# Performance work log

Measured on AMD Instinct MI355X. Metric: run time of the kernel, lower is better.

Reference implementation:

```python
import jax, jax.numpy as jnp
import numpy as np
from jax import lax

EPS = 1e-5

def _conv(x, w, stride, padding):
    # x: NCHW, w: OIHW
    return lax.conv_general_dilated(
        x, w, window_strides=(stride, stride), padding=padding,
        dimension_numbers=("NCHW", "OIHW", "NCHW"))

def _bn(x, gamma, beta):
    # BatchNorm2d in training mode: batch statistics over (N, H, W)
    mean = jnp.mean(x, axis=(0, 2, 3), keepdims=True)
    var = jnp.var(x, axis=(0, 2, 3), keepdims=True)
    inv = lax.rsqrt(var + EPS)
    g = gamma.reshape(1, -1, 1, 1)
    b = beta.reshape(1, -1, 1, 1)
    return (x - mean) * inv * g + b

def setup_inputs() -> dict:
    key = jax.random.key(0)
    ks = jax.random.split(key, 5)
    B, Cin, H, W = 128, 64, 56, 56
    Cout = 128
    x = jax.random.normal(ks[0], (B, Cin, H, W), dtype=jnp.float32)
    w1 = jax.random.normal(ks[1], (Cout, Cin, 3, 3), dtype=jnp.float32) * 0.05
    w2 = jax.random.normal(ks[2], (Cout, Cout, 3, 3), dtype=jnp.float32) * 0.05
    wd = jax.random.normal(ks[3], (Cout, Cin, 1, 1), dtype=jnp.float32) * 0.05
    g1 = jnp.ones((Cout,), jnp.float32); b1 = jnp.zeros((Cout,), jnp.float32)
    g2 = jnp.ones((Cout,), jnp.float32); b2 = jnp.zeros((Cout,), jnp.float32)
    gd = jnp.ones((Cout,), jnp.float32); bd = jnp.zeros((Cout,), jnp.float32)
    return {"x": x, "w1": w1, "g1": g1, "b1": b1,
            "w2": w2, "g2": g2, "b2": b2,
            "wd": wd, "gd": gd, "bd": bd}

def reference(x, w1, g1, b1, w2, g2, b2, wd, gd, bd):
    stride = 2
    # conv1 (3x3, stride=2, 'same') -> BN -> ReLU
    out = _conv(x, w1, stride, "SAME")
    out = jax.nn.relu(_bn(out, g1, b1))
    # conv2 (3x3, stride=1, 'same') -> BN
    out = _conv(out, w2, 1, "SAME")
    out = _bn(out, g2, b2)
    # downsample identity: 1x1 conv stride=2 'valid' -> BN
    identity = _bn(_conv(x, wd, stride, "VALID"), gd, bd)
    return jax.nn.relu(out + identity)
```

## Files before the change

kernel.cpp:

```cpp
#include <hip/hip_runtime.h>

constexpr int B = 128, Cin = 64, H = 56, W = 56;
constexpr int Cout = 128, Ho = 28, Wo = 28;
constexpr int HW = Ho * Wo;
constexpr int NPIX = B * HW;
constexpr int NOUT = NPIX * Cout;
constexpr int NBLK2 = NPIX / 256;
constexpr float EPS_ = 1e-5f;
constexpr float CNT_ = (float)NPIX;

constexpr int HPX = 57, WPX = 57;
constexpr int HP1 = 30, WP1 = 30;

typedef __attribute__((ext_vector_type(8))) unsigned short u16x8;
typedef __attribute__((ext_vector_type(4))) unsigned short u16x4;
typedef __attribute__((ext_vector_type(8))) short bf16x8;
typedef __attribute__((ext_vector_type(4))) float f32x4;

__device__ inline float bf2f(unsigned short u) {
    union { unsigned int i; float f; } v; v.i = ((unsigned int)u) << 16; return v.f;
}
__device__ inline unsigned short f2bf(float f) {
    union { float f; unsigned int i; } v; v.f = f;
    return (unsigned short)((v.i + 0x7fffu + ((v.i >> 16) & 1u)) >> 16);
}

__device__ inline void gload16(const void* g, void* l) {
    __builtin_amdgcn_global_load_lds(
        (const __attribute__((address_space(1))) unsigned int*)g,
        (__attribute__((address_space(3))) unsigned int*)l, 16, 0, 0);
}

__global__ __launch_bounds__(512) void k_conv2_mfma(
        const unsigned short* __restrict__ xin,
        const unsigned short* __restrict__ wt,
        unsigned short* __restrict__ yout,
        float* __restrict__ part) {
    constexpr int CIN = 128, WP = 30, KTOT = 1152, NSTEP = 36;
    __shared__ unsigned short Alds[3][256 * 32];
    __shared__ unsigned short Blds[3][128 * 32];
    __shared__ float lsum[8][64], lsq[8][64];
    const int tid = threadIdx.x, w = tid >> 6, l = tid & 63;
    const int wr = w >> 1, wc = w & 1;
    const int bid = (blockIdx.x & 7) * (NBLK2 / 8) + (blockIdx.x >> 3);
    const int p0 = bid * 256;
    const char* xb = (const char*)xin;
    const char* wb = (const char*)wt;

    const int sslot = ((l & 3) ^ ((l >> 3) & 3)) * 16;
    const int rswz  = ((l >> 4) ^ ((l >> 1) & 3)) * 16;

    int gA[2], lofsA[2];
    #pragma unroll
    for (int i = 0; i < 2; ++i) {
        int row = w * 32 + i * 16 + (l >> 2);
        int p = p0 + row;
        int n = p / HW, rr = p % HW;
        int oh = rr / Wo, ow = rr % Wo;
        gA[i] = (((n * HP1 + oh) * WP + ow) * CIN) * 2 + sslot;
        lofsA[i] = row * 64 + (l & 3) * 16;
    }
    const int rowb = w * 16 + (l >> 2);
    const int gB = rowb * KTOT * 2 + sslot;
    const int lofsB = rowb * 64 + (l & 3) * 16;

    f32x4 acc[4][4];
    #pragma unroll
    for (int m = 0; m < 4; ++m)
        #pragma unroll
        for (int n = 0; n < 4; ++n)
            acc[m][n] = (f32x4){0.f, 0.f, 0.f, 0.f};

    gload16(xb + gA[0],      (char*)Alds[0] + lofsA[0]);
    gload16(xb + gA[1],      (char*)Alds[0] + lofsA[1]);
    gload16(wb + gB,         (char*)Blds[0] + lofsB);
    gload16(xb + gA[0] + 64, (char*)Alds[1] + lofsA[0]);
    gload16(xb + gA[1] + 64, (char*)Alds[1] + lofsA[1]);
    gload16(wb + gB + 64,    (char*)Blds[1] + lofsB);

    for (int oi = 0; oi < 3; ++oi) {
        const int Abase = oi * WP * CIN * 2;
        #pragma unroll
        for (int u = 0; u < 12; ++u) {
            const int s = oi * 12 + u;
            const int cur = u % 3;
            if (s + 1 < NSTEP) asm volatile("s_waitcnt vmcnt(3)" ::: "memory");
            else               asm volatile("s_waitcnt vmcnt(0)" ::: "memory");
            __builtin_amdgcn_s_barrier();
            if (s + 2 < NSTEP) {
                const int u2 = u + 2;
                const int j2 = u2 >> 2;
                const int c2 = u2 & 3;
                const int koffA = Abase + (j2 == 3 ? WP * CIN * 2 : j2 * CIN * 2) + c2 * 64;
                const int koffB = (s + 2) * 64;
                const int buf = u2 % 3;
                gload16(xb + gA[0] + koffA, (char*)Alds[buf] + lofsA[0]);
                gload16(xb + gA[1] + koffA, (char*)Alds[buf] + lofsA[1]);
                gload16(wb + gB + koffB,    (char*)Blds[buf] + lofsB);
            }
            bf16x8 bf[4];
            #pragma unroll
            for (int n = 0; n < 4; ++n)
                bf[n] = *(const bf16x8*)((const char*)Blds[cur] + (wc * 64 + n * 16 + (l & 15)) * 64 + rswz);
            #pragma unroll
            for (int m = 0; m < 4; ++m) {
                bf16x8 af = *(const bf16x8*)((const char*)Alds[cur] + (wr * 64 + m * 16 + (l & 15)) * 64 + rswz);
                #pragma unroll
                for (int n = 0; n < 4; ++n)
                    acc[m][n] = __builtin_amdgcn_mfma_f32_16x16x32_bf16(af, bf[n], acc[m][n], 0, 0, 0);
            }
        }
    }

    #pragma unroll
    for (int m = 0; m < 4; ++m) {
        int pq = p0 + wr * 64 + m * 16 + (l >> 4) * 4;
        int n = pq / HW, rr = pq % HW;
        #pragma unroll
        for (int q = 0; q < 4; ++q) {
            int co = wc * 64 + q * 16 + (l & 15);
            u16x4 v;
            #pragma unroll
            for (int r = 0; r < 4; ++r) v[r] = f2bf(acc[m][q][r]);
            *(u16x4*)(yout + ((size_t)(n * Cout + co)) * HW + rr) = v;
        }
    }

    float ps[4], pq_[4];
    #pragma unroll
    for (int n = 0; n < 4; ++n) {
        float s_ = 0.f, q_ = 0.f;
        #pragma unroll
        for (int m = 0; m < 4; ++m)
            #pragma unroll
            for (int r = 0; r < 4; ++r) { float v = acc[m][n][r]; s_ += v; q_ += v * v; }
        s_ += __shfl_xor(s_, 16); q_ += __shfl_xor(q_, 16);
        s_ += __shfl_xor(s_, 32); q_ += __shfl_xor(q_, 32);
        ps[n] = s_; pq_[n] = q_;
    }
    __syncthreads();
    if (l < 16) {
        #pragma unroll
        for (int n = 0; n < 4; ++n) { lsum[w][n * 16 + l] = ps[n]; lsq[w][n * 16 + l] = pq_[n]; }
    }
    __syncthreads();
    if (tid < 128) {
        int c = tid, half = c >> 6, j = c & 63;
        float s_ = 0.f, q_ = 0.f;
        #pragma unroll
        for (int r = 0; r < 4; ++r) { s_ += lsum[r * 2 + half][j]; q_ += lsq[r * 2 + half][j]; }
        part[((size_t)bid * 128 + c) * 2]     = s_;
        part[((size_t)bid * 128 + c) * 2 + 1] = q_;
    }
}

__global__ __launch_bounds__(512) void k_conv1_mfma(
        const unsigned short* __restrict__ xin,
        const unsigned short* __restrict__ wt,
        const unsigned short* __restrict__ wtd,
        unsigned short* __restrict__ yout,
        unsigned short* __restrict__ ydout,
        float* __restrict__ part, float* __restrict__ partd) {
    constexpr int CIN = 64, WP = 57, KTOT = 576, NSTEP = 18;
    __shared__ unsigned short Alds[3][256 * 32];
    __shared__ unsigned short Blds[3][128 * 32];
    __shared__ float lsum[8][64], lsq[8][64];
    const int tid = threadIdx.x, w = tid >> 6, l = tid & 63;
    const int wr = w >> 1, wc = w & 1;
    const int bid = (blockIdx.x & 7) * (NBLK2 / 8) + (blockIdx.x >> 3);
    const int p0 = bid * 256;
    const char* xb = (const char*)xin;
    const char* wb = (const char*)wt;

    const int sslot = ((l & 3) ^ ((l >> 3) & 3)) * 16;
    const int rswz  = ((l >> 4) ^ ((l >> 1) & 3)) * 16;

    int gA[2], lofsA[2];
    #pragma unroll
    for (int i = 0; i < 2; ++i) {
        int row = w * 32 + i * 16 + (l >> 2);
        int p = p0 + row;
        int n = p / HW, rr = p % HW;
        int oh = rr / Wo, ow = rr % Wo;
        gA[i] = (((n * HPX + oh * 2) * WP + ow * 2) * CIN) * 2 + sslot;
        lofsA[i] = row * 64 + (l & 3) * 16;
    }
    const int rowb = w * 16 + (l >> 2);
    const int gB = rowb * KTOT * 2 + sslot;
    const int lofsB = rowb * 64 + (l & 3) * 16;

    bf16x8 bd[2][4];
    #pragma unroll
    for (int s = 0; s < 2; ++s)
        #pragma unroll
        for (int n = 0; n < 4; ++n) {
            int co = wc * 64 + n * 16 + (l & 15);
            bd[s][n] = *(const bf16x8*)(wtd + co * 64 + s * 32 + (l >> 4) * 8);
        }

    f32x4 acc[4][4], accd[4][4];
    #pragma unroll
    for (int m = 0; m < 4; ++m)
        #pragma unroll
        for (int n = 0; n < 4; ++n) {
            acc[m][n]  = (f32x4){0.f, 0.f, 0.f, 0.f};
            accd[m][n] = (f32x4){0.f, 0.f, 0.f, 0.f};
        }

    #pragma unroll
    for (int s = 0; s < 2; ++s) {
        gload16(xb + gA[0] + s * 64, (char*)Alds[s] + lofsA[0]);
        gload16(xb + gA[1] + s * 64, (char*)Alds[s] + lofsA[1]);
        gload16(wb + gB + s * 64,    (char*)Blds[s] + lofsB);
    }

    #pragma unroll
    for (int s = 0; s < NSTEP; ++s) {
        const int cur = s % 3;
        if (s + 1 < NSTEP) asm volatile("s_waitcnt vmcnt(3)" ::: "memory");
        else               asm volatile("s_waitcnt vmcnt(0)" ::: "memory");
        __builtin_amdgcn_s_barrier();
        if (s + 2 < NSTEP) {
            const int s2 = s + 2;
            const int seg = s2 >> 1, kh = seg / 3, kw = seg % 3;
            const int koffA = (kh * WP + kw) * CIN * 2 + (s2 & 1) * 64;
            const int koffB = s2 * 64;
            const int buf = s2 % 3;
            gload16(xb + gA[0] + koffA, (char*)Alds[buf] + lofsA[0]);
            gload16(xb + gA[1] + koffA, (char*)Alds[buf] + lofsA[1]);
            gload16(wb + gB + koffB,    (char*)Blds[buf] + lofsB);
        }
        bf16x8 bf[4];
        #pragma unroll
        for (int n = 0; n < 4; ++n)
            bf[n] = *(const bf16x8*)((const char*)Blds[cur] + (wc * 64 + n * 16 + (l & 15)) * 64 + rswz);
        #pragma unroll
        for (int m = 0; m < 4; ++m) {
            bf16x8 af = *(const bf16x8*)((const char*)Alds[cur] + (wr * 64 + m * 16 + (l & 15)) * 64 + rswz);
            #pragma unroll
            for (int n = 0; n < 4; ++n)
                acc[m][n] = __builtin_amdgcn_mfma_f32_16x16x32_bf16(af, bf[n], acc[m][n], 0, 0, 0);
            if (s < 2) {
                #pragma unroll
                for (int n = 0; n < 4; ++n)
                    accd[m][n] = __builtin_amdgcn_mfma_f32_16x16x32_bf16(af, bd[s][n], accd[m][n], 0, 0, 0);
            }
        }
    }

    #pragma unroll
    for (int m = 0; m < 4; ++m) {
        #pragma unroll
        for (int r = 0; r < 4; ++r) {
            int p = p0 + wr * 64 + m * 16 + (l >> 4) * 4 + r;
            int n = p / HW, rr = p % HW;
            int oh = rr / Wo, ow = rr % Wo;
            unsigned short* dst = yout + ((size_t)((n * HP1 + oh + 1) * WP1 + ow + 1)) * 128
                                 + wc * 64 + (l & 15);
            #pragma unroll
            for (int q = 0; q < 4; ++q)
                dst[q * 16] = f2bf(acc[m][q][r]);
        }
    }
    #pragma unroll
    for (int m = 0; m < 4; ++m) {
        int pq = p0 + wr * 64 + m * 16 + (l >> 4) * 4;
        int n = pq / HW, rr = pq % HW;
        #pragma unroll
        for (int q = 0; q < 4; ++q) {
            int co = wc * 64 + q * 16 + (l & 15);
            u16x4 v;
            #pragma unroll
            for (int r = 0; r < 4; ++r) v[r] = f2bf(accd[m][q][r]);
            *(u16x4*)(ydout + ((size_t)(n * Cout + co)) * HW + rr) = v;
        }
    }

    #pragma unroll
    for (int pass = 0; pass < 2; ++pass) {
        f32x4 (&a)[4][4] = pass ? accd : acc;
        float* pt = pass ? partd : part;
        float ps[4], pq_[4];
        #pragma unroll
        for (int n = 0; n < 4; ++n) {
            float s_ = 0.f, q_ = 0.f;
            #pragma unroll
            for (int m = 0; m < 4; ++m)
                #pragma unroll
                for (int r = 0; r < 4; ++r) { float v = a[m][n][r]; s_ += v; q_ += v * v; }
            s_ += __shfl_xor(s_, 16); q_ += __shfl_xor(q_, 16);
            s_ += __shfl_xor(s_, 32); q_ += __shfl_xor(q_, 32);
            ps[n] = s_; pq_[n] = q_;
        }
        __syncthreads();
        if (l < 16) {
            #pragma unroll
            for (int n = 0; n < 4; ++n) { lsum[w][n * 16 + l] = ps[n]; lsq[w][n * 16 + l] = pq_[n]; }
        }
        __syncthreads();
        if (tid < 128) {
            int c = tid, half = c >> 6, j = c & 63;
            float s_ = 0.f, q_ = 0.f;
            #pragma unroll
            for (int r = 0; r < 4; ++r) { s_ += lsum[r * 2 + half][j]; q_ += lsq[r * 2 + half][j]; }
            pt[((size_t)bid * 128 + c) * 2]     = s_;
            pt[((size_t)bid * 128 + c) * 2 + 1] = q_;
        }
    }
}

__global__ __launch_bounds__(256) void k_zerob(unsigned short* __restrict__ xb,
                                               unsigned short* __restrict__ y1p) {
    int idx = blockIdx.x * 256 + threadIdx.x;
    constexpr int NA = B * 113 * 8;
    const u16x8 z = (u16x8){0, 0, 0, 0, 0, 0, 0, 0};
    if (idx < NA) {
        int cg = idx & 7; int t = idx >> 3;
        int bp = t % 113, n = t / 113;
        int ih = bp < 57 ? 56 : bp - 57;
        int iw = bp < 57 ? bp : 56;
        *(u16x8*)(xb + ((size_t)((n * HPX + ih) * WPX + iw)) * Cin + cg * 8) = z;
    } else {
        idx -= NA;
        if (idx >= B * 116 * 16) return;
        int cg = idx & 15; int t = idx >> 4;
        int bp = t % 116, n = t / 116;
        int oh, ow;
        if (bp < 30)      { oh = 0;           ow = bp; }
        else if (bp < 60) { oh = 29;          ow = bp - 30; }
        else if (bp < 88) { oh = bp - 60 + 1; ow = 0; }
        else              { oh = bp - 88 + 1; ow = 29; }
        *(u16x8*)(y1p + ((size_t)((n * HP1 + oh) * WP1 + ow)) * 128 + cg * 8) = z;
    }
}

__global__ __launch_bounds__(512) void k_xprep(const float* __restrict__ x,
                                               unsigned short* __restrict__ xb) {
    __shared__ unsigned short lds[2][64 * 57];
    int n = blockIdx.x / (H / 2), ihp = blockIdx.x % (H / 2), ih0 = ihp * 2;
    const float* src = x + ((size_t)n * Cin * H + ih0) * W;
    for (int j = threadIdx.x; j < 2 * Cin * 14; j += 512) {
        int r = j / 896, rem = j % 896;
        int c = rem / 14, q = rem % 14;
        float4 v = *(const float4*)(src + ((size_t)c * H + r) * W + q * 4);
        unsigned short* d = &lds[r][c * 57 + q * 4];
        d[0] = f2bf(v.x); d[1] = f2bf(v.y); d[2] = f2bf(v.z); d[3] = f2bf(v.w);
    }
    __syncthreads();
    for (int k = threadIdx.x; k < 2 * W * 8; k += 512) {
        int r = k / 448, k2 = k % 448;
        int pix = k2 >> 3, cg = k2 & 7;
        u16x8 v;
        #pragma unroll
        for (int e = 0; e < 8; ++e) v[e] = lds[r][(cg * 8 + e) * 57 + pix];
        *(u16x8*)(xb + ((size_t)((n * HPX + ih0 + r) * WPX + pix)) * Cin + cg * 8) = v;
    }
}

__global__ void k_wprep_all(const float* __restrict__ w1, const float* __restrict__ w2,
                            const float* __restrict__ wd,
                            unsigned short* __restrict__ wt1, unsigned short* __restrict__ wt2,
                            unsigned short* __restrict__ wtd) {
    int idx = blockIdx.x * 256 + threadIdx.x;
    const float* w; unsigned short* wt; int cin, ntap;
    if (idx < 73728)            { w = w1; wt = wt1; cin = 64;  ntap = 9; }
    else if (idx < 73728 + 147456) { idx -= 73728; w = w2; wt = wt2; cin = 128; ntap = 9; }
    else if (idx < 73728 + 147456 + 8192) { idx -= 73728 + 147456; w = wd; wt = wtd; cin = 64; ntap = 1; }
    else return;
    int co = idx / (cin * ntap), r = idx % (cin * ntap);
    int ci = r / ntap, tap = r % ntap;
    wt[co * cin * ntap + tap * cin + ci] = f2bf(w[idx]);
}

__device__ inline void block_reduce2(float& s, float& s2) {
    #pragma unroll
    for (int off = 32; off > 0; off >>= 1) {
        s += __shfl_down(s, off);
        s2 += __shfl_down(s2, off);
    }
    __shared__ float ls[4], ls2[4];
    int wid = threadIdx.x >> 6, lane = threadIdx.x & 63;
    if (lane == 0) { ls[wid] = s; ls2[wid] = s2; }
    __syncthreads();
    if (threadIdx.x == 0) { s = ls[0] + ls[1] + ls[2] + ls[3]; s2 = ls2[0] + ls2[1] + ls2[2] + ls2[3]; }
}

__global__ __launch_bounds__(256) void k_finalize(
        const float* __restrict__ pA, const float* __restrict__ pB, int nA, int nB,
        const float* __restrict__ gA_, const float* __restrict__ bA_,
        const float* __restrict__ gB_, const float* __restrict__ bB_,
        float* __restrict__ scA, float* __restrict__ shA,
        float* __restrict__ scB, float* __restrict__ shB) {
    const bool second = blockIdx.x >= 128;
    const int c = blockIdx.x & 127;
    const float* part = second ? pB : pA;
    const int nblk = second ? nB : nA;
    const float* g = second ? gB_ : gA_;
    const float* b = second ? bB_ : bA_;
    float* scale = second ? scB : scA;
    float* shift = second ? shB : shA;
    float s = 0.f, q = 0.f;
    for (int k = threadIdx.x; k < nblk; k += 256) {
        s += part[((size_t)k * 128 + c) * 2];
        q += part[((size_t)k * 128 + c) * 2 + 1];
    }
    block_reduce2(s, q);
    if (threadIdx.x == 0) {
        float mean = s / CNT_;
        float var = q / CNT_ - mean * mean;
        float inv = rsqrtf(var + EPS_);
        scale[c] = g[c] * inv;
        shift[c] = b[c] - mean * g[c] * inv;
    }
}

__global__ __launch_bounds__(256) void k_bnrelu(unsigned short* __restrict__ y,
        const float* __restrict__ sc, const float* __restrict__ sh) {
    int t = threadIdx.x, cg = t & 15, pl = t >> 4;
    int p = blockIdx.x * 16 + pl;
    int n = p / HW, rr = p % HW;
    int oh = rr / Wo, ow = rr % Wo;
    size_t a = ((size_t)((n * HP1 + oh + 1) * WP1 + ow + 1)) * 128 + cg * 8;
    u16x8 v = *(u16x8*)(y + a);
    u16x8 o;
    #pragma unroll
    for (int e = 0; e < 8; ++e) {
        float f = bf2f(v[e]) * sc[cg * 8 + e] + sh[cg * 8 + e];
        o[e] = f2bf(fmaxf(f, 0.f));
    }
    *(u16x8*)(y + a) = o;
}

__global__ __launch_bounds__(256) void k_final(
        const unsigned short* __restrict__ y2, const unsigned short* __restrict__ yd,
        const float* __restrict__ sc2, const float* __restrict__ sh2,
        const float* __restrict__ scd, const float* __restrict__ shd,
        float* __restrict__ out) {
    int idx = blockIdx.x * 256 + threadIdx.x;
    int plane = idx / (HW / 8);
    int c = plane & (Cout - 1);
    int i = idx % (HW / 8);
    size_t a = (size_t)plane * HW + i * 8;
    u16x8 v2 = *(const u16x8*)(y2 + a);
    u16x8 vd = *(const u16x8*)(yd + a);
    float s2c = sc2[c], h2c = sh2[c], sdc = scd[c], hdc = shd[c];
    float4 r0, r1;
    r0.x = fmaxf(bf2f(v2[0]) * s2c + h2c + bf2f(vd[0]) * sdc + hdc, 0.f);
    r0.y = fmaxf(bf2f(v2[1]) * s2c + h2c + bf2f(vd[1]) * sdc + hdc, 0.f);
    r0.z = fmaxf(bf2f(v2[2]) * s2c + h2c + bf2f(vd[2]) * sdc + hdc, 0.f);
    r0.w = fmaxf(bf2f(v2[3]) * s2c + h2c + bf2f(vd[3]) * sdc + hdc, 0.f);
    r1.x = fmaxf(bf2f(v2[4]) * s2c + h2c + bf2f(vd[4]) * sdc + hdc, 0.f);
    r1.y = fmaxf(bf2f(v2[5]) * s2c + h2c + bf2f(vd[5]) * sdc + hdc, 0.f);
    r1.z = fmaxf(bf2f(v2[6]) * s2c + h2c + bf2f(vd[6]) * sdc + hdc, 0.f);
    r1.w = fmaxf(bf2f(v2[7]) * s2c + h2c + bf2f(vd[7]) * sdc + hdc, 0.f);
    *(float4*)(out + a) = r0;
    *(float4*)(out + a + 4) = r1;
}

extern "C" void kernel_launch(void* const* d_in, const int* in_sizes, int n_in,
                              void* d_out, int out_size, void* d_ws, size_t ws_size,
                              hipStream_t stream) {
    const float* x  = (const float*)d_in[0];
    const float* w1 = (const float*)d_in[1];
    const float* g1 = (const float*)d_in[2];
    const float* b1 = (const float*)d_in[3];
    const float* w2 = (const float*)d_in[4];
    const float* g2 = (const float*)d_in[5];
    const float* b2 = (const float*)d_in[6];
    const float* wd = (const float*)d_in[7];
    const float* gd = (const float*)d_in[8];
    const float* bd = (const float*)d_in[9];
    float* out = (float*)d_out;

    char* ws = (char*)d_ws;
    auto alloc = [&](size_t bytes) { char* p = ws; ws += (bytes + 255) & ~(size_t)255; return p; };
    unsigned short* xb  = (unsigned short*)alloc((size_t)B * HPX * WPX * Cin * 2);
    unsigned short* y1p = (unsigned short*)alloc((size_t)B * HP1 * WP1 * Cout * 2);
    unsigned short* y2b = (unsigned short*)alloc((size_t)NOUT * 2);
    unsigned short* ydb = (unsigned short*)alloc((size_t)NOUT * 2);
    unsigned short* wt1 = (unsigned short*)alloc((size_t)Cout * 576 * 2);
    unsigned short* wt2 = (unsigned short*)alloc((size_t)Cout * 1152 * 2);
    unsigned short* wtd = (unsigned short*)alloc((size_t)Cout * 64 * 2);
    float* part1 = (float*)alloc((size_t)NBLK2 * 128 * 2 * 4);
    float* part2 = (float*)alloc((size_t)NBLK2 * 128 * 2 * 4);
    float* partd = (float*)alloc((size_t)NBLK2 * 128 * 2 * 4);
    float* sc1 = (float*)alloc(128 * 4); float* sh1 = (float*)alloc(128 * 4);
    float* sc2 = (float*)alloc(128 * 4); float* sh2 = (float*)alloc(128 * 4);
    float* scd = (float*)alloc(128 * 4); float* shd = (float*)alloc(128 * 4);

    k_zerob<<<(B * 113 * 8 + B * 116 * 16 + 255) / 256, 256, 0, stream>>>(xb, y1p);
    k_xprep<<<B * (H / 2), 512, 0, stream>>>(x, xb);
    k_wprep_all<<<(73728 + 147456 + 8192 + 255) / 256, 256, 0, stream>>>(w1, w2, wd, wt1, wt2, wtd);

    k_conv1_mfma<<<NBLK2, 512, 0, stream>>>(xb, wt1, wtd, y1p, ydb, part1, partd);

    k_finalize<<<128, 256, 0, stream>>>(part1, part1, NBLK2, NBLK2,
                                        g1, b1, g1, b1, sc1, sh1, sc1, sh1);
    k_bnrelu<<<NPIX / 16, 256, 0, stream>>>(y1p, sc1, sh1);

    k_conv2_mfma<<<NBLK2, 512, 0, stream>>>(y1p, wt2, y2b, part2);

    k_finalize<<<256, 256, 0, stream>>>(part2, partd, NBLK2, NBLK2,
                                        g2, b2, gd, bd, sc2, sh2, scd, shd);

    k_final<<<NOUT / 8 / 256, 256, 0, stream>>>(y2b, ydb, sc2, sh2, scd, shd, out);
}
```

Measured before the change: 164.3 us.

## Raise MFMA wave priority, merge prep kernels, widen elementwise kernels

Wraps the MFMA inner loops of both conv kernels in s_setprio(1)/s_setprio(0), so waves issuing matrix ops get scheduling priority over waves doing loads. Merges the zero-border and weight-prep kernels into one launch to drop a kernel launch. The BN+ReLU and final epilogue kernels now handle 16 elements per thread instead of 8, halving their grid sizes. These are several small independent tweaks, and priority changes can hurt the overlap of loads and compute.

```diff
diff --git a/kernel.cpp b/kernel.cpp
--- a/kernel.cpp
+++ b/kernel.cpp
@@ -102,6 +102,7 @@
             #pragma unroll
             for (int n = 0; n < 4; ++n)
                 bf[n] = *(const bf16x8*)((const char*)Blds[cur] + (wc * 64 + n * 16 + (l & 15)) * 64 + rswz);
+            __builtin_amdgcn_s_setprio(1);
             #pragma unroll
             for (int m = 0; m < 4; ++m) {
                 bf16x8 af = *(const bf16x8*)((const char*)Alds[cur] + (wr * 64 + m * 16 + (l & 15)) * 64 + rswz);
@@ -109,6 +110,7 @@
                 for (int n = 0; n < 4; ++n)
                     acc[m][n] = __builtin_amdgcn_mfma_f32_16x16x32_bf16(af, bf[n], acc[m][n], 0, 0, 0);
             }
+            __builtin_amdgcn_s_setprio(0);
         }
     }
 
@@ -234,6 +236,7 @@
         #pragma unroll
         for (int n = 0; n < 4; ++n)
             bf[n] = *(const bf16x8*)((const char*)Blds[cur] + (wc * 64 + n * 16 + (l & 15)) * 64 + rswz);
+        __builtin_amdgcn_s_setprio(1);
         #pragma unroll
         for (int m = 0; m < 4; ++m) {
             bf16x8 af = *(const bf16x8*)((const char*)Alds[cur] + (wr * 64 + m * 16 + (l & 15)) * 64 + rswz);
@@ -246,6 +249,7 @@
                     accd[m][n] = __builtin_amdgcn_mfma_f32_16x16x32_bf16(af, bd[s][n], accd[m][n], 0, 0, 0);
             }
         }
+        __builtin_amdgcn_s_setprio(0);
     }
 
     #pragma unroll
@@ -309,20 +313,25 @@
     }
 }
 
-__global__ __launch_bounds__(256) void k_zerob(unsigned short* __restrict__ xb,
-                                               unsigned short* __restrict__ y1p) {
+constexpr int NZA = B * 113 * 8;
+constexpr int NZB = B * 116 * 16;
+constexpr int NWP = 73728 + 147456 + 8192;
+__global__ __launch_bounds__(256) void k_prep(
+        unsigned short* __restrict__ xb, unsigned short* __restrict__ y1p,
+        const float* __restrict__ w1, const float* __restrict__ w2,
+        const float* __restrict__ wd,
+        unsigned short* __restrict__ wt1, unsigned short* __restrict__ wt2,
+        unsigned short* __restrict__ wtd) {
     int idx = blockIdx.x * 256 + threadIdx.x;
-    constexpr int NA = B * 113 * 8;
     const u16x8 z = (u16x8){0, 0, 0, 0, 0, 0, 0, 0};
-    if (idx < NA) {
+    if (idx < NZA) {
         int cg = idx & 7; int t = idx >> 3;
         int bp = t % 113, n = t / 113;
         int ih = bp < 57 ? 56 : bp - 57;
         int iw = bp < 57 ? bp : 56;
         *(u16x8*)(xb + ((size_t)((n * HPX + ih) * WPX + iw)) * Cin + cg * 8) = z;
-    } else {
-        idx -= NA;
-        if (idx >= B * 116 * 16) return;
+    } else if (idx < NZA + NZB) {
+        idx -= NZA;
         int cg = idx & 15; int t = idx >> 4;
         int bp = t % 116, n = t / 116;
         int oh, ow;
@@ -331,6 +340,16 @@
         else if (bp < 88) { oh = bp - 60 + 1; ow = 0; }
         else              { oh = bp - 88 + 1; ow = 29; }
         *(u16x8*)(y1p + ((size_t)((n * HP1 + oh) * WP1 + ow)) * 128 + cg * 8) = z;
+    } else {
+        idx -= NZA + NZB;
+        if (idx >= NWP) return;
+        const float* w; unsigned short* wt; int cin, ntap;
+        if (idx < 73728)               { w = w1; wt = wt1; cin = 64;  ntap = 9; }
+        else if (idx < 73728 + 147456) { idx -= 73728; w = w2; wt = wt2; cin = 128; ntap = 9; }
+        else                           { idx -= 73728 + 147456; w = wd; wt = wtd; cin = 64; ntap = 1; }
+        int co = idx / (cin * ntap), r = idx % (cin * ntap);
+        int ci = r / ntap, tap = r % ntap;
+        wt[co * cin * ntap + tap * cin + ci] = f2bf(w[idx]);
     }
 }
 
@@ -355,21 +374,6 @@
         for (int e = 0; e < 8; ++e) v[e] = lds[r][(cg * 8 + e) * 57 + pix];
         *(u16x8*)(xb + ((size_t)((n * HPX + ih0 + r) * WPX + pix)) * Cin + cg * 8) = v;
     }
-}
-
-__global__ void k_wprep_all(const float* __restrict__ w1, const float* __restrict__ w2,
-                            const float* __restrict__ wd,
-                            unsigned short* __restrict__ wt1, unsigned short* __restrict__ wt2,
-                            unsigned short* __restrict__ wtd) {
-    int idx = blockIdx.x * 256 + threadIdx.x;
-    const float* w; unsigned short* wt; int cin, ntap;
-    if (idx < 73728)            { w = w1; wt = wt1; cin = 64;  ntap = 9; }
-    else if (idx < 73728 + 147456) { idx -= 73728; w = w2; wt = wt2; cin = 128; ntap = 9; }
-    else if (idx < 73728 + 147456 + 8192) { idx -= 73728 + 147456; w = wd; wt = wtd; cin = 64; ntap = 1; }
-    else return;
-    int co = idx / (cin * ntap), r = idx % (cin * ntap);
-    int ci = r / ntap, tap = r % ntap;
-    wt[co * cin * ntap + tap * cin + ci] = f2bf(w[idx]);
 }
 
 __device__ inline void block_reduce2(float& s, float& s2) {
@@ -416,19 +420,23 @@
 
 __global__ __launch_bounds__(256) void k_bnrelu(unsigned short* __restrict__ y,
         const float* __restrict__ sc, const float* __restrict__ sh) {
-    int t = threadIdx.x, cg = t & 15, pl = t >> 4;
-    int p = blockIdx.x * 16 + pl;
+    int t = threadIdx.x, cg = t & 7, pl = t >> 3;
+    int p = blockIdx.x * 32 + pl;
     int n = p / HW, rr = p % HW;
     int oh = rr / Wo, ow = rr % Wo;
-    size_t a = ((size_t)((n * HP1 + oh + 1) * WP1 + ow + 1)) * 128 + cg * 8;
-    u16x8 v = *(u16x8*)(y + a);
-    u16x8 o;
+    size_t a = ((size_t)((n * HP1 + oh + 1) * WP1 + ow + 1)) * 128 + cg * 16;
+    u16x8 v0 = *(u16x8*)(y + a);
+    u16x8 v1 = *(u16x8*)(y + a + 8);
+    u16x8 o0, o1;
     #pragma unroll
     for (int e = 0; e < 8; ++e) {
-        float f = bf2f(v[e]) * sc[cg * 8 + e] + sh[cg * 8 + e];
-        o[e] = f2bf(fmaxf(f, 0.f));
-    }
-    *(u16x8*)(y + a) = o;
+        float f0 = bf2f(v0[e]) * sc[cg * 16 + e] + sh[cg * 16 + e];
+        float f1 = bf2f(v1[e]) * sc[cg * 16 + 8 + e] + sh[cg * 16 + 8 + e];
+        o0[e] = f2bf(fmaxf(f0, 0.f));
+        o1[e] = f2bf(fmaxf(f1, 0.f));
+    }
+    *(u16x8*)(y + a) = o0;
+    *(u16x8*)(y + a + 8) = o1;
 }
 
 __global__ __launch_bounds__(256) void k_final(
@@ -436,25 +444,28 @@
         const float* __restrict__ sc2, const float* __restrict__ sh2,
         const float* __restrict__ scd, const float* __restrict__ shd,
         float* __restrict__ out) {
-    int idx = blockIdx.x * 256 + threadIdx.x;
-    int plane = idx / (HW / 8);
+    int u = blockIdx.x * 256 + threadIdx.x;
+    int plane = u / 49;
     int c = plane & (Cout - 1);
-    int i = idx % (HW / 8);
-    size_t a = (size_t)plane * HW + i * 8;
-    u16x8 v2 = *(const u16x8*)(y2 + a);
-    u16x8 vd = *(const u16x8*)(yd + a);
+    int i = u % 49;
+    size_t a = (size_t)plane * HW + i * 16;
     float s2c = sc2[c], h2c = sh2[c], sdc = scd[c], hdc = shd[c];
-    float4 r0, r1;
-    r0.x = fmaxf(bf2f(v2[0]) * s2c + h2c + bf2f(vd[0]) * sdc + hdc, 0.f);
-    r0.y = fmaxf(bf2f(v2[1]) * s2c + h2c + bf2f(vd[1]) * sdc + hdc, 0.f);
-    r0.z = fmaxf(bf2f(v2[2]) * s2c + h2c + bf2f(vd[2]) * sdc + hdc, 0.f);
-    r0.w = fmaxf(bf2f(v2[3]) * s2c + h2c + bf2f(vd[3]) * sdc + hdc, 0.f);
-    r1.x = fmaxf(bf2f(v2[4]) * s2c + h2c + bf2f(vd[4]) * sdc + hdc, 0.f);
-    r1.y = fmaxf(bf2f(v2[5]) * s2c + h2c + bf2f(vd[5]) * sdc + hdc, 0.f);
-    r1.z = fmaxf(bf2f(v2[6]) * s2c + h2c + bf2f(vd[6]) * sdc + hdc, 0.f);
-    r1.w = fmaxf(bf2f(v2[7]) * s2c + h2c + bf2f(vd[7]) * sdc + hdc, 0.f);
-    *(float4*)(out + a) = r0;
-    *(float4*)(out + a + 4) = r1;
+    #pragma unroll
+    for (int hv = 0; hv < 2; ++hv) {
+        u16x8 v2 = *(const u16x8*)(y2 + a + hv * 8);
+        u16x8 vd = *(const u16x8*)(yd + a + hv * 8);
+        float4 r0, r1;
+        r0.x = fmaxf(bf2f(v2[0]) * s2c + h2c + bf2f(vd[0]) * sdc + hdc, 0.f);
+        r0.y = fmaxf(bf2f(v2[1]) * s2c + h2c + bf2f(vd[1]) * sdc + hdc, 0.f);
+        r0.z = fmaxf(bf2f(v2[2]) * s2c + h2c + bf2f(vd[2]) * sdc + hdc, 0.f);
+        r0.w = fmaxf(bf2f(v2[3]) * s2c + h2c + bf2f(vd[3]) * sdc + hdc, 0.f);
+        r1.x = fmaxf(bf2f(v2[4]) * s2c + h2c + bf2f(vd[4]) * sdc + hdc, 0.f);
+        r1.y = fmaxf(bf2f(v2[5]) * s2c + h2c + bf2f(vd[5]) * sdc + hdc, 0.f);
+        r1.z = fmaxf(bf2f(v2[6]) * s2c + h2c + bf2f(vd[6]) * sdc + hdc, 0.f);
+        r1.w = fmaxf(bf2f(v2[7]) * s2c + h2c + bf2f(vd[7]) * sdc + hdc, 0.f);
+        *(float4*)(out + a + hv * 8)     = r0;
+        *(float4*)(out + a + hv * 8 + 4) = r1;
+    }
 }
 
 extern "C" void kernel_launch(void* const* d_in, const int* in_sizes, int n_in,
@@ -488,20 +499,20 @@
     float* sc2 = (float*)alloc(128 * 4); float* sh2 = (float*)alloc(128 * 4);
     float* scd = (float*)alloc(128 * 4); float* shd = (float*)alloc(128 * 4);
 
-    k_zerob<<<(B * 113 * 8 + B * 116 * 16 + 255) / 256, 256, 0, stream>>>(xb, y1p);
+    k_prep<<<(NZA + NZB + NWP + 255) / 256, 256, 0, stream>>>(
+        xb, y1p, w1, w2, wd, wt1, wt2, wtd);
     k_xprep<<<B * (H / 2), 512, 0, stream>>>(x, xb);
-    k_wprep_all<<<(73728 + 147456 + 8192 + 255) / 256, 256, 0, stream>>>(w1, w2, wd, wt1, wt2, wtd);
 
     k_conv1_mfma<<<NBLK2, 512, 0, stream>>>(xb, wt1, wtd, y1p, ydb, part1, partd);
 
     k_finalize<<<128, 256, 0, stream>>>(part1, part1, NBLK2, NBLK2,
                                         g1, b1, g1, b1, sc1, sh1, sc1, sh1);
-    k_bnrelu<<<NPIX / 16, 256, 0, stream>>>(y1p, sc1, sh1);
+    k_bnrelu<<<NPIX / 32, 256, 0, stream>>>(y1p, sc1, sh1);
 
     k_conv2_mfma<<<NBLK2, 512, 0, stream>>>(y1p, wt2, y2b, part2);
 
     k_finalize<<<256, 256, 0, stream>>>(part2, partd, NBLK2, NBLK2,
                                         g2, b2, gd, bd, sc2, sh2, scd, shd);
 
-    k_final<<<NOUT / 8 / 256, 256, 0, stream>>>(y2b, ydb, sc2, sh2, scd, shd, out);
-}
+    k_final<<<NOUT / 16 / 256, 256, 0, stream>>>(y2b, ydb, sc2, sh2, scd, shd, out);
+}
```

New measurement: 182.2 us. 1.11x slower.
